# Kernel tuning notes

Measured on AMD Instinct MI355X. Metric: run time of the kernel, lower is better.

Reference implementation:

```python
import jax, jax.numpy as jnp
import numpy as np

N_NODES = 100000
N_EDGES = 3200000
F = 32          # n_node_features
L = 50          # n_node_labels
EL = 10         # n_edge_labels
K = 16          # out_dim (graph_data.num_classes)


def setup_inputs() -> dict:
    key = jax.random.key(0)
    ks = jax.random.split(key, 12)
    x = jax.random.normal(ks[0], (N_NODES, F), dtype=jnp.float32)
    node_labels = jax.random.randint(ks[1], (N_NODES,), 0, L, dtype=jnp.int32)
    edge_src = jax.random.randint(ks[2], (N_EDGES,), 0, N_NODES, dtype=jnp.int32)
    edge_dst = jax.random.randint(ks[3], (N_EDGES,), 0, N_NODES, dtype=jnp.int32)
    edge_labels = jax.random.randint(ks[4], (N_EDGES,), 0, EL, dtype=jnp.int32)
    s = 0.1
    W1 = jax.random.normal(ks[5], (L, L, EL), dtype=jnp.float32) * s
    b1 = jax.random.normal(ks[6], (L,), dtype=jnp.float32) * s
    W2 = jax.random.normal(ks[7], (L, L, EL), dtype=jnp.float32) * s
    b2 = jax.random.normal(ks[8], (L,), dtype=jnp.float32) * s
    W3 = jax.random.normal(ks[9], (L, L, EL), dtype=jnp.float32) * s
    b3 = jax.random.normal(ks[10], (L,), dtype=jnp.float32) * s
    kr1, kr2 = jax.random.split(ks[11])
    Wr = jax.random.normal(kr1, (L, F, K), dtype=jnp.float32) * s
    br = jax.random.normal(kr2, (K,), dtype=jnp.float32) * s
    return {"x": x, "W1": W1, "b1": b1, "W2": W2, "b2": b2, "W3": W3, "b3": b3,
            "Wr": Wr, "br": br, "node_labels": node_labels,
            "edge_src": edge_src, "edge_dst": edge_dst, "edge_labels": edge_labels}


def _conv(x, W, b, node_labels, edge_src, edge_dst, edge_labels):
    # weight_rule_wf: per-edge scalar weight indexed by (src label, dst label, edge label)
    w_e = W[node_labels[edge_src], node_labels[edge_dst], edge_labels]  # [E]
    msgs = w_e[:, None] * x[edge_src]                                   # [E, F]
    agg = jax.ops.segment_sum(msgs, edge_dst, num_segments=x.shape[0])  # [N, F]
    # node_label_rule bias: per-node bias indexed by node label, then Tanh
    return jnp.tanh(agg + b[node_labels][:, None])


def reference(x, W1, b1, W2, b2, W3, b3, Wr, br,
              node_labels, edge_src, edge_dst, edge_labels):
    h = _conv(x, W1, b1, node_labels, edge_src, edge_dst, edge_labels)
    h = _conv(h, W2, b2, node_labels, edge_src, edge_dst, edge_labels)
    h = _conv(h, W3, b3, node_labels, edge_src, edge_dst, edge_labels)
    # GraphResizeLayer (node_label_rule): out[k] = sum_i Wr[label_i, f, k] * h[i, f] + br[k]
    # equivalent efficient form: pre-aggregate node features by label, then contract.
    sums = jax.ops.segment_sum(h, node_labels, num_segments=Wr.shape[0])  # [L, F]
    out = jnp.tanh(jnp.einsum('lf,lfk->k', sums, Wr) + br)                # [K]
    return out
```

## Files before the change

kernel.cpp:

```cpp
#include <hip/hip_runtime.h>
#include <hip/hip_bf16.h>
#include <hip/hip_fp8.h>

#define NN 100000
#define NE 3200000
#define FF 32
#define LL 50
#define ELB 10
#define KK 16

#define CH 8192
#define NBLK_P1 391
#define NBUK 196
#define CAP 18432

typedef float floatx2 __attribute__((ext_vector_type(2)));

__device__ __forceinline__ float fast_tanh(float x) {
    float e = __expf(2.0f * x);
    return 1.0f - 2.0f / (e + 1.0f);
}

__global__ __launch_bounds__(512) void p1_scatter(const int* __restrict__ esrc,
                                                  const int* __restrict__ edst,
                                                  const int* __restrict__ elab,
                                                  const float* __restrict__ x,
                                                  unsigned* __restrict__ xb,
                                                  int* __restrict__ cursor,
                                                  unsigned* __restrict__ recs) {
    __shared__ int lcnt[NBUK];
    __shared__ int lbase[NBUK];
    int tid = threadIdx.x;
    for (int i = blockIdx.x * 512 + tid; i < NN * FF / 4; i += NBLK_P1 * 512) {
        float4 v = ((const float4*)x)[i];
        __hip_fp8_e4m3 a(v.x), b(v.y), c(v.z), d(v.w);
        xb[i] = (unsigned)a.__x | ((unsigned)b.__x << 8) |
                ((unsigned)c.__x << 16) | ((unsigned)d.__x << 24);
    }
    for (int i = tid; i < NBUK; i += 512) lcnt[i] = 0;
    __syncthreads();
    long e0 = (long)blockIdx.x * CH;
    long rem = NE - e0;
    int cnt = rem < CH ? (int)rem : CH;
    int nq = cnt >> 2;
    const int4* edst4 = (const int4*)(edst + e0);
    const int4* esrc4 = (const int4*)(esrc + e0);
    const int4* elab4 = (const int4*)(elab + e0);
    for (int i = tid; i < nq; i += 512) {
        int4 d = edst4[i];
        atomicAdd(&lcnt[d.x >> 9], 1);
        atomicAdd(&lcnt[d.y >> 9], 1);
        atomicAdd(&lcnt[d.z >> 9], 1);
        atomicAdd(&lcnt[d.w >> 9], 1);
    }
    __syncthreads();
    for (int i = tid; i < NBUK; i += 512) {
        int c = lcnt[i];
        lbase[i] = c ? atomicAdd(&cursor[i], c) : 0;
        lcnt[i] = 0;
    }
    __syncthreads();
    for (int i = tid; i < nq; i += 512) {
        int4 s4 = esrc4[i];
        int4 l4 = elab4[i];
        int4 d4 = edst4[i];
#pragma unroll
        for (int k = 0; k < 4; ++k) {
            int s  = (&s4.x)[k];
            int d  = (&d4.x)[k];
            int el = (&l4.x)[k];
            int b = d >> 9;
            int ofs = atomicAdd(&lcnt[b], 1);
            int rel = lbase[b] + ofs;
            if (rel < CAP)
                recs[b * CAP + rel] =
                    ((unsigned)s << 13) | ((unsigned)el << 9) | (unsigned)(d & 511);
        }
    }
}

__global__ __launch_bounds__(512) void p2_local(const int* __restrict__ cursor,
                                                const unsigned* __restrict__ recs,
                                                const int* __restrict__ labels,
                                                unsigned* __restrict__ packed,
                                                int* __restrict__ gstart,
                                                int* __restrict__ gcnt) {
    __shared__ int deg[512], loff[512], lcur[512], sc[512], labd[512];
    int b = blockIdx.x, tid = threadIdx.x;
    int base = b * CAP;
    int n = cursor[b];
    if (n > CAP) n = CAP;
    int node = (b << 9) + tid;
    deg[tid] = 0;
    lcur[tid] = 0;
    labd[tid] = (node < NN) ? labels[node] : 0;
    __syncthreads();
    for (int i = tid; i < n; i += 512)
        atomicAdd(&deg[(int)(recs[base + i] & 511)], 1);
    __syncthreads();
    sc[tid] = deg[tid];
    __syncthreads();
    for (int ofs = 1; ofs < 512; ofs <<= 1) {
        int t = (tid >= ofs) ? sc[tid - ofs] : 0;
        __syncthreads();
        sc[tid] += t;
        __syncthreads();
    }
    loff[tid] = sc[tid] - deg[tid];
    if (node < NN) { gstart[node] = base + loff[tid]; gcnt[node] = deg[tid]; }
    __syncthreads();
    for (int i = tid; i < n; i += 512) {
        unsigned r = recs[base + i];
        int dl  = (int)(r & 511);
        int el  = (int)((r >> 9) & 15);
        int src = (int)(r >> 13);
        int widx = labels[src] * (LL * ELB) + labd[dl] * ELB + el;
        int ofs = atomicAdd(&lcur[dl], 1);
        packed[base + loff[dl] + ofs] = ((unsigned)widx << 17) | (unsigned)src;
    }
}

__global__ __launch_bounds__(256) void conv_kernel(const unsigned char* __restrict__ xin,
                                                   unsigned char* __restrict__ hout,
                                                   const int* __restrict__ gstart,
                                                   const int* __restrict__ gcnt,
                                                   const unsigned* __restrict__ packed,
                                                   const float* __restrict__ Wtab,
                                                   const float* __restrict__ bias,
                                                   const int* __restrict__ labels) {
    __shared__ unsigned stage[8][64];
    int tid = threadIdx.x;
    int hw = tid >> 5, lane = tid & 31;
    int node = (blockIdx.x << 3) + hw;
    int s = gstart[node];
    int n = gcnt[node];
    int eg = lane >> 3;
    int fg = (lane & 7) << 2;
    float4 acc = {0.f, 0.f, 0.f, 0.f};
    for (int base = 0; base < n; base += 32) {
        float w = 0.f;
        unsigned so = 0u;
        int idx = base + lane;
        if (idx < n) {
            unsigned p = packed[s + idx];
            w = Wtab[p >> 17];
            so = (p & 0x1FFFFu) << 5;
        }
        ((uint2*)&stage[hw][0])[lane] = make_uint2(__float_as_uint(w), so);
        __builtin_amdgcn_wave_barrier();
#pragma unroll
        for (int j = 0; j < 8; ++j) {
            uint2 ws = ((const uint2*)&stage[hw][0])[j * 4 + eg];
            unsigned pv = *(const unsigned*)(xin + ws.y + fg);
            floatx2 lo = __builtin_amdgcn_cvt_pk_f32_fp8((int)pv, false);
            floatx2 hi = __builtin_amdgcn_cvt_pk_f32_fp8((int)pv, true);
            float we = __uint_as_float(ws.x);
            acc.x += we * lo.x;
            acc.y += we * lo.y;
            acc.z += we * hi.x;
            acc.w += we * hi.y;
        }
        __builtin_amdgcn_wave_barrier();
    }
    acc.x += __shfl_xor(acc.x, 8);  acc.y += __shfl_xor(acc.y, 8);
    acc.z += __shfl_xor(acc.z, 8);  acc.w += __shfl_xor(acc.w, 8);
    acc.x += __shfl_xor(acc.x, 16); acc.y += __shfl_xor(acc.y, 16);
    acc.z += __shfl_xor(acc.z, 16); acc.w += __shfl_xor(acc.w, 16);
    if (lane < 8) {
        float bb = bias[labels[node]];
        __hip_fp8_e4m3 q0(fast_tanh(acc.x + bb));
        __hip_fp8_e4m3 q1(fast_tanh(acc.y + bb));
        __hip_fp8_e4m3 q2(fast_tanh(acc.z + bb));
        __hip_fp8_e4m3 q3(fast_tanh(acc.w + bb));
        unsigned pk = (unsigned)q0.__x | ((unsigned)q1.__x << 8) |
                      ((unsigned)q2.__x << 16) | ((unsigned)q3.__x << 24);
        ((unsigned*)(hout + ((long)node << 5)))[lane] = pk;
    }
}

__global__ __launch_bounds__(256) void lsum_resize_kernel(const unsigned* __restrict__ h,
                                                          const int* __restrict__ labels,
                                                          float* __restrict__ sums,
                                                          int* __restrict__ done,
                                                          const float* __restrict__ Wr,
                                                          const float* __restrict__ br,
                                                          float* __restrict__ out) {
    __shared__ float ls[LL * FF];
    __shared__ int winner;
    int tid = threadIdx.x;
    for (int i = tid; i < LL * FF; i += 256) ls[i] = 0.f;
    __syncthreads();
    for (int i = blockIdx.x * 256 + tid; i < NN * 8; i += gridDim.x * 256) {
        unsigned pv = h[i];
        int nodei = i >> 3;
        int fb = (i & 7) << 2;
        int l = labels[nodei];
        floatx2 lo = __builtin_amdgcn_cvt_pk_f32_fp8((int)pv, false);
        floatx2 hi = __builtin_amdgcn_cvt_pk_f32_fp8((int)pv, true);
        float* bp = &ls[l * FF + fb];
        atomicAdd(bp + 0, lo.x);
        atomicAdd(bp + 1, lo.y);
        atomicAdd(bp + 2, hi.x);
        atomicAdd(bp + 3, hi.y);
    }
    __syncthreads();
    for (int i = tid; i < LL * FF; i += 256) atomicAdd(&sums[i], ls[i]);
    __threadfence();
    if (tid == 0) winner = (atomicAdd(done, 1) == (int)gridDim.x - 1) ? 1 : 0;
    __syncthreads();
    if (!winner) return;
    __shared__ float red[256][KK];
    float acc[KK];
#pragma unroll
    for (int k = 0; k < KK; ++k) acc[k] = 0.f;
    for (int p = tid; p < LL * FF; p += 256) {
        float sv = atomicAdd(&sums[p], 0.0f);
#pragma unroll
        for (int k = 0; k < KK; ++k) acc[k] += sv * Wr[p * KK + k];
    }
#pragma unroll
    for (int k = 0; k < KK; ++k) red[tid][k] = acc[k];
    __syncthreads();
    for (int sft = 128; sft > 0; sft >>= 1) {
        if (tid < sft) {
#pragma unroll
            for (int k = 0; k < KK; ++k) red[tid][k] += red[tid + sft][k];
        }
        __syncthreads();
    }
    if (tid < KK) out[tid] = fast_tanh(red[0][tid] + br[tid]);
}

extern "C" void kernel_launch(void* const* d_in, const int* in_sizes, int n_in,
                              void* d_out, int out_size, void* d_ws, size_t ws_size,
                              hipStream_t stream) {
    const float* x   = (const float*)d_in[0];
    const float* W1  = (const float*)d_in[1];
    const float* b1  = (const float*)d_in[2];
    const float* W2  = (const float*)d_in[3];
    const float* b2  = (const float*)d_in[4];
    const float* W3  = (const float*)d_in[5];
    const float* b3  = (const float*)d_in[6];
    const float* Wr  = (const float*)d_in[7];
    const float* br  = (const float*)d_in[8];
    const int* labels = (const int*)d_in[9];
    const int* esrc   = (const int*)d_in[10];
    const int* edst   = (const int*)d_in[11];
    const int* elab   = (const int*)d_in[12];
    float* out = (float*)d_out;

    char* ws = (char*)d_ws;
    size_t o = 0;
    auto alloc = [&](size_t bytes) -> void* {
        void* p = ws + o;
        o += (bytes + 255) & ~(size_t)255;
        return p;
    };
    char* regionA = (char*)alloc((size_t)NBUK * CAP * sizeof(unsigned));
    unsigned* recs = (unsigned*)regionA;
    unsigned char* h1 = (unsigned char*)regionA;
    unsigned char* h2 = (unsigned char*)(regionA + (size_t)NN * FF);

    unsigned* packed = (unsigned*)alloc((size_t)NBUK * CAP * sizeof(unsigned));
    unsigned* xb     = (unsigned*)alloc((size_t)NN * FF);
    int* cursor = (int*)alloc(NBUK * sizeof(int));
    float* sums = (float*)alloc(LL * FF * sizeof(float));
    int* done   = (int*)alloc(sizeof(int));
    int* gstart = (int*)alloc(NN * sizeof(int));
    int* gcnt   = (int*)alloc(NN * sizeof(int));

    size_t msz = (size_t)((char*)done - (char*)cursor) + sizeof(int);
    hipMemsetAsync(cursor, 0, msz, stream);

    p1_scatter<<<NBLK_P1, 512, 0, stream>>>(esrc, edst, elab, x, xb, cursor, recs);
    p2_local<<<NBUK, 512, 0, stream>>>(cursor, recs, labels, packed, gstart, gcnt);

    conv_kernel<<<NN / 8, 256, 0, stream>>>((const unsigned char*)xb, h1, gstart, gcnt, packed, W1, b1, labels);
    conv_kernel<<<NN / 8, 256, 0, stream>>>(h1, h2, gstart, gcnt, packed, W2, b2, labels);
    conv_kernel<<<NN / 8, 256, 0, stream>>>(h2, h1, gstart, gcnt, packed, W3, b3, labels);

    lsum_resize_kernel<<<128, 256, 0, stream>>>((const unsigned*)h1, labels, sums, done, Wr, br, out);
}
```

Before: 321.8 us.

## Privatize label sums per half-wave and contract with Wr in every block

The final label-sum and resize kernel now gives each 32-lane half-wave its own shared-memory label histogram, so the per-node accumulation needs no LDS atomics. Each block then contracts its partial sums with Wr locally and atomically adds only 16 outputs to global memory, instead of 1600 sums followed by a serial last-block contraction. The grid grows to 256 blocks of 512 threads and uses about 100KB of shared memory per block. The final tail is much smaller, but every block now reads Wr.

```diff
diff --git a/kernel.cpp b/kernel.cpp
--- a/kernel.cpp
+++ b/kernel.cpp
@@ -13,6 +13,8 @@
 #define NBLK_P1 391
 #define NBUK 196
 #define CAP 18432
+
+#define LSB 256
 
 typedef float floatx2 __attribute__((ext_vector_type(2)));
 
@@ -178,57 +180,65 @@
     }
 }
 
-__global__ __launch_bounds__(256) void lsum_resize_kernel(const unsigned* __restrict__ h,
-                                                          const int* __restrict__ labels,
-                                                          float* __restrict__ sums,
-                                                          int* __restrict__ done,
-                                                          const float* __restrict__ Wr,
-                                                          const float* __restrict__ br,
-                                                          float* __restrict__ out) {
-    __shared__ float ls[LL * FF];
+__global__ __launch_bounds__(512, 1) void lsum_resize_kernel(
+        const unsigned* __restrict__ h32,
+        const int* __restrict__ labels,
+        const float* __restrict__ Wr,
+        const float* __restrict__ br,
+        float* __restrict__ outacc,
+        int* __restrict__ done,
+        float* __restrict__ out) {
+    __shared__ float ls[16][LL * FF];
+    __shared__ float po[KK];
     __shared__ int winner;
     int tid = threadIdx.x;
-    for (int i = tid; i < LL * FF; i += 256) ls[i] = 0.f;
-    __syncthreads();
-    for (int i = blockIdx.x * 256 + tid; i < NN * 8; i += gridDim.x * 256) {
-        unsigned pv = h[i];
-        int nodei = i >> 3;
-        int fb = (i & 7) << 2;
-        int l = labels[nodei];
-        floatx2 lo = __builtin_amdgcn_cvt_pk_f32_fp8((int)pv, false);
-        floatx2 hi = __builtin_amdgcn_cvt_pk_f32_fp8((int)pv, true);
-        float* bp = &ls[l * FF + fb];
-        atomicAdd(bp + 0, lo.x);
-        atomicAdd(bp + 1, lo.y);
-        atomicAdd(bp + 2, hi.x);
-        atomicAdd(bp + 3, hi.y);
-    }
-    __syncthreads();
-    for (int i = tid; i < LL * FF; i += 256) atomicAdd(&sums[i], ls[i]);
+    int hw = tid >> 5, lane = tid & 31;
+    for (int i = tid; i < 16 * LL * FF; i += 512) ((float*)ls)[i] = 0.f;
+    if (tid < KK) po[tid] = 0.f;
+    __syncthreads();
+    int widx = lane >> 2;
+    int bsh  = (lane & 3) << 3;
+    float* myls = &ls[hw][0];
+    for (int node = blockIdx.x * 16 + hw; node < NN; node += LSB * 16) {
+        unsigned wv = h32[node * 8 + widx];
+        floatx2 vv = __builtin_amdgcn_cvt_pk_f32_fp8((int)(wv >> bsh), false);
+        float v = vv.x;
+        int l = labels[node];
+        myls[l * FF + lane] += v;
+    }
+    __syncthreads();
+    float pk[KK];
+#pragma unroll
+    for (int k = 0; k < KK; ++k) pk[k] = 0.f;
+    for (int e = tid; e < LL * FF; e += 512) {
+        float s = 0.f;
+#pragma unroll
+        for (int c = 0; c < 16; ++c) s += ls[c][e];
+        const float* wr = Wr + e * KK;
+#pragma unroll
+        for (int k = 0; k < KK; ++k) pk[k] += s * wr[k];
+    }
+#pragma unroll
+    for (int k = 0; k < KK; ++k) {
+        pk[k] += __shfl_xor(pk[k], 1);
+        pk[k] += __shfl_xor(pk[k], 2);
+        pk[k] += __shfl_xor(pk[k], 4);
+        pk[k] += __shfl_xor(pk[k], 8);
+        pk[k] += __shfl_xor(pk[k], 16);
+        pk[k] += __shfl_xor(pk[k], 32);
+    }
+    if ((tid & 63) == 0) {
+#pragma unroll
+        for (int k = 0; k < KK; ++k) atomicAdd(&po[k], pk[k]);
+    }
+    __syncthreads();
+    if (tid < KK) atomicAdd(&outacc[tid], po[tid]);
     __threadfence();
-    if (tid == 0) winner = (atomicAdd(done, 1) == (int)gridDim.x - 1) ? 1 : 0;
-    __syncthreads();
-    if (!winner) return;
-    __shared__ float red[256][KK];
-    float acc[KK];
-#pragma unroll
-    for (int k = 0; k < KK; ++k) acc[k] = 0.f;
-    for (int p = tid; p < LL * FF; p += 256) {
-        float sv = atomicAdd(&sums[p], 0.0f);
-#pragma unroll
-        for (int k = 0; k < KK; ++k) acc[k] += sv * Wr[p * KK + k];
-    }
-#pragma unroll
-    for (int k = 0; k < KK; ++k) red[tid][k] = acc[k];
-    __syncthreads();
-    for (int sft = 128; sft > 0; sft >>= 1) {
-        if (tid < sft) {
-#pragma unroll
-            for (int k = 0; k < KK; ++k) red[tid][k] += red[tid + sft][k];
-        }
-        __syncthreads();
-    }
-    if (tid < KK) out[tid] = fast_tanh(red[0][tid] + br[tid]);
+    __syncthreads();
+    if (tid == 0) winner = (atomicAdd(done, 1) == LSB - 1) ? 1 : 0;
+    __syncthreads();
+    if (winner && tid < KK)
+        out[tid] = fast_tanh(atomicAdd(&outacc[tid], 0.0f) + br[tid]);
 }
 
 extern "C" void kernel_launch(void* const* d_in, const int* in_sizes, int n_in,
@@ -263,14 +273,14 @@
 
     unsigned* packed = (unsigned*)alloc((size_t)NBUK * CAP * sizeof(unsigned));
     unsigned* xb     = (unsigned*)alloc((size_t)NN * FF);
-    int* cursor = (int*)alloc(NBUK * sizeof(int));
-    float* sums = (float*)alloc(LL * FF * sizeof(float));
-    int* done   = (int*)alloc(sizeof(int));
-    int* gstart = (int*)alloc(NN * sizeof(int));
-    int* gcnt   = (int*)alloc(NN * sizeof(int));
+    int* cursor   = (int*)alloc(NBUK * sizeof(int));
+    float* outacc = (float*)alloc(KK * sizeof(float));
+    int* done     = (int*)alloc(sizeof(int));
+    int* gstart   = (int*)alloc(NN * sizeof(int));
+    int* gcnt     = (int*)alloc(NN * sizeof(int));
 
     size_t msz = (size_t)((char*)done - (char*)cursor) + sizeof(int);
-    hipMemsetAsync(cursor, 0, msz, stream);
+    (void)hipMemsetAsync(cursor, 0, msz, stream);
 
     p1_scatter<<<NBLK_P1, 512, 0, stream>>>(esrc, edst, elab, x, xb, cursor, recs);
     p2_local<<<NBUK, 512, 0, stream>>>(cursor, recs, labels, packed, gstart, gcnt);
@@ -279,5 +289,6 @@
     conv_kernel<<<NN / 8, 256, 0, stream>>>(h1, h2, gstart, gcnt, packed, W2, b2, labels);
     conv_kernel<<<NN / 8, 256, 0, stream>>>(h2, h1, gstart, gcnt, packed, W3, b3, labels);
 
-    lsum_resize_kernel<<<128, 256, 0, stream>>>((const unsigned*)h1, labels, sums, done, Wr, br, out);
-}
+    lsum_resize_kernel<<<LSB, 512, 0, stream>>>((const unsigned*)h1, labels, Wr, br,
+                                                outacc, done, out);
+}
```

Measured after the change: 319.1 us. Within noise of the previous version (-0.9%).
